# Performance work log

Hardware: AMD Instinct MI355X
Metric: run time of the kernel (lower is better)

Reference implementation:

```python
import jax, jax.numpy as jnp
import numpy as np

WIN = 7            # window side -> K2 = 49
DIM = 512          # channel dim C
HEADS = 16
E = DIM // HEADS   # embed_dim / head_dim = 32
SCALE = E ** -0.5


def _rel_pos_index(wh, ww):
    coords = np.stack(np.meshgrid(np.arange(wh), np.arange(ww), indexing='ij'))  # [2, wh, ww]
    cf = coords.reshape(2, -1)                      # [2, K2]
    rel = cf[:, :, None] - cf[:, None, :]           # [2, K2, K2]
    rel = rel.transpose(1, 2, 0).astype(np.int64)   # [K2, K2, 2]
    rel[..., 0] += wh - 1
    rel[..., 1] += ww - 1
    rel[..., 0] *= 2 * ww - 1
    return rel.sum(-1)                              # [K2, K2]

RPI = jnp.asarray(_rel_pos_index(WIN, WIN))         # constant int index map


def setup_inputs() -> dict:
    key = jax.random.key(0)
    ks = jax.random.split(key, 9)
    s = 0.02
    return {
        'x':         jax.random.normal(ks[0], (2048, WIN * WIN, DIM), jnp.float32),
        'qk_w':      jax.random.normal(ks[1], (2 * DIM, DIM), jnp.float32) * s,
        'qk_b':      jnp.zeros((2 * DIM,), jnp.float32),
        'rev_v_w':   jax.random.normal(ks[2], (DIM, DIM), jnp.float32) * s,
        'rev_v_b':   jnp.zeros((DIM,), jnp.float32),
        'wg_w':      jax.random.normal(ks[3], (E * E, DIM), jnp.float32) * s,
        'proj_w':    jax.random.normal(ks[4], (DIM, DIM), jnp.float32) * s,
        'proj_b':    jnp.zeros((DIM,), jnp.float32),
        'rpb_table': jax.random.normal(ks[5], ((2 * WIN - 1) ** 2, HEADS), jnp.float32) * s,
    }


def reference(x, qk_w, qk_b, rev_v_w, rev_v_b, wg_w, proj_w, proj_b, rpb_table):
    BW, K2, C = x.shape
    # joint q/k projection: [BW, K2, 2, H, E]
    qk = (x @ qk_w.T + qk_b).reshape(BW, K2, 2, HEADS, E)
    q = qk[:, :, 0].transpose(0, 2, 1, 3) * SCALE   # [BW, H, K2, E]
    k = qk[:, :, 1].transpose(0, 2, 1, 3)           # [BW, H, K2, E]
    attn = jnp.einsum('bhqe,bhke->bhqk', q, k)      # [BW, H, K2, K2]
    # relative position bias gather: [K2, K2, H] -> [H, K2, K2]
    bias = rpb_table[RPI].transpose(2, 0, 1)
    attn = jax.nn.softmax(attn + bias[None], axis=-1)
    # reverse attention: values projected, softmax transposed (transpose_softmax=True)
    v = (x @ rev_v_w.T + rev_v_b).reshape(BW, K2, HEADS, E).transpose(0, 2, 1, 3)  # [BW, H, K2, E]
    expert_mixture = jnp.einsum('bhkq,bhke->bhqe', attn, v)   # attn^T @ v, [BW, H, K2, E]
    # hypernetwork: per-token E x E mixing matrices from the raw input
    proj_weight = (x @ wg_w.T).reshape(BW, K2, E, E)          # [BW, K2, E, E]
    em_t = expert_mixture.transpose(0, 2, 1, 3)               # [BW, K2, H, E]
    out = jnp.einsum('bkhe,bkef->bkhf', em_t, proj_weight).reshape(BW, K2, C)
    # output projection (reverse_proj); dropouts are identity (p=0)
    return out @ proj_w.T + proj_b
```

## Files before the change

### kernel.cpp

```cpp
#include <hip/hip_runtime.h>
#include <hip/hip_bf16.h>
#include <stdint.h>

typedef __attribute__((ext_vector_type(8))) short short8;
typedef __attribute__((ext_vector_type(4))) float f32x4;
typedef unsigned short u16;

#define SCALE_F 0.17677669529663687f

__device__ __forceinline__ u16 f2bf(float f){
  union { float f; unsigned u; } x; x.f = f;
  unsigned r = x.u + 0x7fffu + ((x.u >> 16) & 1u);
  return (u16)(r >> 16);
}
__device__ __forceinline__ float bf2f(u16 u){
  union { float f; unsigned u; } x; x.u = ((unsigned)u) << 16; return x.f;
}
__device__ __forceinline__ unsigned swz(unsigned base, int row, unsigned rowb, unsigned colb){
  return base + (unsigned)row * rowb + (colb ^ (((unsigned)row & 7u) << 4));
}
__device__ __forceinline__ void gll16(const void* g, void* l){
  __builtin_amdgcn_global_load_lds(
    (const __attribute__((address_space(1))) unsigned int*)(unsigned long long)(size_t)g,
    (__attribute__((address_space(3))) unsigned int*)(unsigned int)(size_t)l,
    16, 0, 0);
}

__global__ void convk(const float* __restrict__ x,
                      const float* __restrict__ qk_w, const float* __restrict__ rev_v_w,
                      const float* __restrict__ wg_w, const float* __restrict__ proj_w,
                      u16* __restrict__ ws){
  long long i8 = ((long long)blockIdx.x * 256 + threadIdx.x) * 8;
  const float* s;
  if      (i8 <  524288) s = qk_w   + i8;
  else if (i8 <  786432) s = rev_v_w + (i8 - 524288);
  else if (i8 < 1310720) s = wg_w   + (i8 - 786432);
  else if (i8 < 1572864) s = proj_w + (i8 - 1310720);
  else                   s = x      + (i8 - 1572864);
  f32x4 lo = *(const f32x4*)s, hi = *(const f32x4*)(s + 4);
  short8 v;
  v[0]=f2bf(lo[0]); v[1]=f2bf(lo[1]); v[2]=f2bf(lo[2]); v[3]=f2bf(lo[3]);
  v[4]=f2bf(hi[0]); v[5]=f2bf(hi[1]); v[6]=f2bf(hi[2]); v[7]=f2bf(hi[3]);
  *(short8*)(ws + i8) = v;
}

template<int NT, int F32OUT>
__global__ __launch_bounds__(256, 2)
void gemm128(const u16* __restrict__ A, int lda,
             const u16* __restrict__ B,
             const float* __restrict__ b0, const float* __restrict__ b1,
             void* __restrict__ Cg, int ldc){
  __shared__ __align__(16) unsigned char sm[32768];
  const int tid = threadIdx.x, wave = tid >> 6, lane = tid & 63;
  const int l15 = lane & 15, lg = lane >> 4;
  const int nwg = gridDim.x, bidr = blockIdx.x;
  const int q8 = nwg >> 3, r8 = nwg & 7, xc = bidr & 7, oo = bidr >> 3;
  const int wg = (xc < r8 ? xc * (q8 + 1) : r8 * (q8 + 1) + (xc - r8) * q8) + oo;
  const int bm = wg / NT, bn = wg % NT;
  const int wm = wave >> 1, wn = wave & 1;
  const f32x4 zf = {0.f, 0.f, 0.f, 0.f};
  f32x4 acc[4][4];
#pragma unroll
  for (int mt=0; mt<4; mt++)
#pragma unroll
    for (int nt=0; nt<4; nt++) acc[mt][nt] = zf;

  const u16* Ab = A + (size_t)bm * 128 * lda;
  const u16* Bb = B + (size_t)bn * 128 * 512;
  const int r0 = ((wave*4)*64 + lane) >> 3;

  for (int ks = 0; ks < 8; ks++){
#pragma unroll
    for (int it = 0; it < 4; it++){
      int c = (wave*4 + it)*64 + lane;
      int r = c >> 3, cc = c & 7;
      int sc = cc ^ (r & 7);
      gll16(Ab + (size_t)r*lda + ks*64 + sc*8, sm + (unsigned)(wave*4 + it)*1024u);
      gll16(Bb + (size_t)r*512 + ks*64 + sc*8, sm + 16384u + (unsigned)(wave*4 + it)*1024u);
    }
    __syncthreads();
#pragma unroll
    for (int kk = 0; kk < 2; kk++){
      short8 aq[4], bq[4];
#pragma unroll
      for (int mt=0; mt<4; mt++){
        int r = wm*64 + mt*16 + l15;
        aq[mt] = *(const short8*)(sm + (unsigned)r*128u + (((unsigned)(kk*64 + lg*16)) ^ (((unsigned)r & 7u) << 4)));
      }
#pragma unroll
      for (int nt=0; nt<4; nt++){
        int r = wn*64 + nt*16 + l15;
        bq[nt] = *(const short8*)(sm + 16384u + (unsigned)r*128u + (((unsigned)(kk*64 + lg*16)) ^ (((unsigned)r & 7u) << 4)));
      }
#pragma unroll
      for (int mt=0; mt<4; mt++)
#pragma unroll
        for (int nt=0; nt<4; nt++)
          acc[mt][nt] = __builtin_amdgcn_mfma_f32_16x16x32_bf16(aq[mt], bq[nt], acc[mt][nt], 0, 0, 0);
    }
    __syncthreads();
  }
  (void)r0;

  float bia[4];
#pragma unroll
  for (int nt=0; nt<4; nt++){
    int n = bn*128 + wn*64 + nt*16 + l15;
    if (F32OUT) bia[nt] = b0[n];
    else        bia[nt] = (n < 1024) ? b0[n] : (n < 1536 ? b1[n - 1024] : 0.f);
  }

  if (!F32OUT){
#pragma unroll
    for (int mt=0; mt<4; mt++)
#pragma unroll
      for (int nt=0; nt<4; nt++)
#pragma unroll
        for (int i=0; i<4; i++){
          int row = wm*64 + mt*16 + lg*4 + i;
          unsigned colb = (unsigned)((wn*64 + nt*16 + l15) * 2);
          *(u16*)(sm + (unsigned)row*256u + (colb ^ (((unsigned)row & 7u) << 4))) = f2bf(acc[mt][nt][i] + bia[nt]);
        }
    __syncthreads();
    u16* Co = (u16*)Cg;
#pragma unroll
    for (int it=0; it<8; it++){
      int c = it*256 + tid;
      int r = c >> 4, cc = c & 15;
      short8 v = *(const short8*)(sm + (unsigned)r*256u + (((unsigned)(cc*16)) ^ (((unsigned)r & 7u) << 4)));
      *(short8*)(Co + (size_t)(bm*128 + r)*ldc + bn*128 + cc*8) = v;
    }
  } else {
    float* Co = (float*)Cg;
#pragma unroll
    for (int half=0; half<2; half++){
      if (wm == half){
#pragma unroll
        for (int mt=0; mt<4; mt++)
#pragma unroll
          for (int nt=0; nt<4; nt++)
#pragma unroll
            for (int i=0; i<4; i++){
              int row = mt*16 + lg*4 + i;
              unsigned colb = (unsigned)((wn*64 + nt*16 + l15) * 4);
              *(float*)(sm + (unsigned)row*512u + (colb ^ (((unsigned)row & 7u) << 4))) = acc[mt][nt][i] + bia[nt];
            }
      }
      __syncthreads();
#pragma unroll
      for (int it=0; it<8; it++){
        int c = it*256 + tid;
        int r = c >> 5, cc = c & 31;
        f32x4 v = *(const f32x4*)(sm + (unsigned)r*512u + (((unsigned)(cc*16)) ^ (((unsigned)r & 7u) << 4)));
        *(f32x4*)(Co + (size_t)(bm*128 + half*64 + r)*ldc + bn*128 + cc*4) = v;
      }
      __syncthreads();
    }
  }
}

__global__ __launch_bounds__(512, 2)
void attn_k(const u16* __restrict__ qkv, const float* __restrict__ rpb,
            u16* __restrict__ em){
  __shared__ __align__(16) unsigned char pt[50176];
  const int tid = threadIdx.x, wave = tid >> 6, lane = tid & 63;
  const int l15 = lane & 15, lg = lane >> 4;
  const size_t wb = (size_t)blockIdx.x * 49;
  const u16* base = qkv + wb * 2560;
  u16* emb = em + wb * 512;
  unsigned char* ptb = pt + (unsigned)wave * 6272u;
  const f32x4 zf = {0.f, 0.f, 0.f, 0.f};

  for (int hp = 0; hp < 2; hp++){
    const int h = wave + hp*8;
    short8 aq[4], bq[4];
#pragma unroll
    for (int mt=0; mt<4; mt++){
      int r = mt*16 + l15; if (r > 48) r = 48;
      aq[mt] = *(const short8*)(base + (size_t)r*2560 + h*32 + lg*8);
    }
#pragma unroll
    for (int nt=0; nt<4; nt++){
      int kt = nt*16 + l15; if (kt > 48) kt = 48;
      bq[nt] = *(const short8*)(base + (size_t)kt*2560 + 512 + h*32 + lg*8);
    }
    f32x4 s[4][4];
#pragma unroll
    for (int mt=0; mt<4; mt++)
#pragma unroll
      for (int nt=0; nt<4; nt++) s[mt][nt] = zf;
#pragma unroll
    for (int mt=0; mt<4; mt++)
#pragma unroll
      for (int nt=0; nt<4; nt++)
        s[mt][nt] = __builtin_amdgcn_mfma_f32_16x16x32_bf16(aq[mt], bq[nt], s[mt][nt], 0, 0, 0);
#pragma unroll
    for (int mt=0; mt<4; mt++)
#pragma unroll
      for (int nt=0; nt<4; nt++)
#pragma unroll
        for (int i=0; i<4; i++){
          int q  = mt*16 + lg*4 + i;
          int kt = nt*16 + l15;
          float v = s[mt][nt][i] * SCALE_F;
          if (kt < 49){
            int qc = (q > 48) ? 48 : q;
            int qi = qc / 7, qj = qc - qi*7;
            int ki = kt / 7, kj = kt - ki*7;
            int idx = (qi - ki + 6)*13 + (qj - kj + 6);
            v += rpb[idx*16 + h];
          } else v = -1e30f;
          s[mt][nt][i] = v;
        }
#pragma unroll
    for (int mt=0; mt<4; mt++)
#pragma unroll
      for (int i=0; i<4; i++){
        float m = fmaxf(fmaxf(s[mt][0][i], s[mt][1][i]), fmaxf(s[mt][2][i], s[mt][3][i]));
        m = fmaxf(m, __shfl_xor(m, 1)); m = fmaxf(m, __shfl_xor(m, 2));
        m = fmaxf(m, __shfl_xor(m, 4)); m = fmaxf(m, __shfl_xor(m, 8));
        float sum = 0.f;
#pragma unroll
        for (int nt=0; nt<4; nt++){ float e = __expf(s[mt][nt][i] - m); s[mt][nt][i] = e; sum += e; }
        sum += __shfl_xor(sum, 1); sum += __shfl_xor(sum, 2);
        sum += __shfl_xor(sum, 4); sum += __shfl_xor(sum, 8);
        float inv = 1.0f / sum;
#pragma unroll
        for (int nt=0; nt<4; nt++) s[mt][nt][i] *= inv;
      }
#pragma unroll
    for (int mt=0; mt<4; mt++)
#pragma unroll
      for (int nt=0; nt<4; nt++)
#pragma unroll
        for (int i=0; i<4; i++){
          int q  = mt*16 + lg*4 + i;
          int kt = nt*16 + l15;
          if (kt < 49){
            u16 val = (q < 49) ? f2bf(s[mt][nt][i]) : (u16)0;
            *(u16*)(ptb + (unsigned)kt*128u + (((unsigned)(q*2)) ^ (((unsigned)kt & 7u) << 4))) = val;
          }
        }
    f32x4 emv[4][2];
#pragma unroll
    for (int mt=0; mt<4; mt++)
#pragma unroll
      for (int nt=0; nt<2; nt++) emv[mt][nt] = zf;
#pragma unroll
    for (int kk=0; kk<2; kk++){
      short8 pa[4];
#pragma unroll
      for (int mt=0; mt<4; mt++){
        int r = mt*16 + l15; if (r > 48) r = 48;
        pa[mt] = *(const short8*)(ptb + (unsigned)r*128u + (((unsigned)(kk*64 + lg*16)) ^ (((unsigned)r & 7u) << 4)));
      }
      short8 vb[2];
#pragma unroll
      for (int nt=0; nt<2; nt++){
        int ch = 1024 + h*32 + nt*16 + l15;
#pragma unroll
        for (int j=0; j<8; j++){
          int kt = kk*32 + lg*8 + j; if (kt > 48) kt = 48;
          vb[nt][j] = *(const short*)(base + (size_t)kt*2560 + ch);
        }
      }
#pragma unroll
      for (int mt=0; mt<4; mt++)
#pragma unroll
        for (int nt=0; nt<2; nt++)
          emv[mt][nt] = __builtin_amdgcn_mfma_f32_16x16x32_bf16(pa[mt], vb[nt], emv[mt][nt], 0, 0, 0);
    }
#pragma unroll
    for (int mt=0; mt<4; mt++)
#pragma unroll
      for (int nt=0; nt<2; nt++)
#pragma unroll
        for (int i=0; i<4; i++){
          int q = mt*16 + lg*4 + i;
          if (q < 49)
            emb[(size_t)q*512 + h*32 + nt*16 + l15] = f2bf(emv[mt][nt][i]);
        }
  }
}

__global__ __launch_bounds__(512, 2)
void hyper_k(const u16* __restrict__ qkvpw, u16* __restrict__ em){
  const int tid = threadIdx.x, wave = tid >> 6, lane = tid & 63;
  const int l15 = lane & 15, lg = lane >> 4;
  const size_t t = (size_t)blockIdx.x * 8 + wave;
  const u16* pwt = qkvpw + t*2560 + 1536;
  u16* emt = em + t*512;
  const f32x4 zf = {0.f, 0.f, 0.f, 0.f};
  short8 ea = *(const short8*)(emt + l15*32 + lg*8);
  f32x4 o[2];
#pragma unroll
  for (int nt=0; nt<2; nt++){
    short8 pb;
#pragma unroll
    for (int j=0; j<8; j++){
      int e = lg*8 + j;
      pb[j] = *(const short*)(pwt + e*32 + nt*16 + l15);
    }
    o[nt] = __builtin_amdgcn_mfma_f32_16x16x32_bf16(ea, pb, zf, 0, 0, 0);
  }
#pragma unroll
  for (int nt=0; nt<2; nt++)
#pragma unroll
    for (int i=0; i<4; i++){
      int h = lg*4 + i;
      emt[h*32 + nt*16 + l15] = f2bf(o[nt][i]);
    }
}

#define LDS_X   0u
#define LDS_V   50176u
#define LDS_QK  100352u
#define LDS_RPB 150528u
#define LDS_PW  50176u
#define LDS_EM  0u
#define LDS_TOTAL 155936

__device__ __forceinline__ void gemm_strip(const unsigned char* ldsp, unsigned abase,
    const u16* __restrict__ W, int wrow0, int l15, int lg, f32x4 acc[4][4]){
  for (int kk = 0; kk < 16; kk++){
    short8 bq[4];
#pragma unroll
    for (int nt = 0; nt < 4; nt++){
      const u16* p = W + (size_t)(wrow0 + nt*16 + l15) * 512 + kk*32 + lg*8;
      bq[nt] = *(const short8*)p;
    }
    short8 aq[4];
#pragma unroll
    for (int mt = 0; mt < 4; mt++){
      int r = mt*16 + l15; if (r > 48) r = 48;
      aq[mt] = *(const short8*)(ldsp + swz(abase, r, 1024u, (unsigned)(kk*64 + lg*16)));
    }
#pragma unroll
    for (int mt = 0; mt < 4; mt++)
#pragma unroll
      for (int nt = 0; nt < 4; nt++)
        acc[mt][nt] = __builtin_amdgcn_mfma_f32_16x16x32_bf16(aq[mt], bq[nt], acc[mt][nt], 0, 0, 0);
  }
}

__global__ void conv_w4(const float* __restrict__ a, const float* __restrict__ b,
                        const float* __restrict__ c, const float* __restrict__ d,
                        u16* __restrict__ o){
  int i = blockIdx.x * 256 + threadIdx.x;
  if (i < 524288)        o[i] = f2bf(a[i]);
  else if (i < 786432)   o[i] = f2bf(b[i - 524288]);
  else if (i < 1310720)  o[i] = f2bf(c[i - 786432]);
  else                   o[i] = f2bf(d[i - 1310720]);
}

__launch_bounds__(512, 2)
__global__ void wa_main(
    const float* __restrict__ x, const float* __restrict__ qk_b,
    const float* __restrict__ rev_v_b, const float* __restrict__ proj_b,
    const float* __restrict__ rpb,
    const u16* __restrict__ Wqk, const u16* __restrict__ Wv,
    const u16* __restrict__ Wwg, const u16* __restrict__ Wproj,
    float* __restrict__ out){
  __shared__ __align__(16) unsigned char ldsp[LDS_TOTAL];
  const int tid  = threadIdx.x;
  const int wave = tid >> 6, lane = tid & 63, l15 = lane & 15, lg = lane >> 4;
  const int b = blockIdx.x;
  const float* xb = x + (size_t)b * 49 * 512;
  const f32x4 zf = {0.f, 0.f, 0.f, 0.f};
  for (int i = tid; i < 169*16; i += 512)
    *(u16*)(ldsp + LDS_RPB + i*2) = f2bf(rpb[i]);
  for (int ch = tid; ch < 49*64; ch += 512){
    int r = ch >> 6, c8 = ch & 63;
    const f32x4* s = (const f32x4*)(xb + r*512 + c8*8);
    f32x4 lo = s[0], hi = s[1];
    short8 v;
    v[0]=f2bf(lo[0]); v[1]=f2bf(lo[1]); v[2]=f2bf(lo[2]); v[3]=f2bf(lo[3]);
    v[4]=f2bf(hi[0]); v[5]=f2bf(hi[1]); v[6]=f2bf(hi[2]); v[7]=f2bf(hi[3]);
    *(short8*)(ldsp + swz(LDS_X, r, 1024u, (unsigned)(c8*16))) = v;
  }
  __syncthreads();
  {
    f32x4 acc[4][4];
#pragma unroll
    for (int mt=0; mt<4; mt++)
#pragma unroll
      for (int nt=0; nt<4; nt++) acc[mt][nt] = zf;
    gemm_strip(ldsp, LDS_X, Wv, wave*64, l15, lg, acc);
#pragma unroll
    for (int nt=0; nt<4; nt++){
      int ch = wave*64 + nt*16 + l15;
      float bias = rev_v_b[ch];
#pragma unroll
      for (int mt=0; mt<4; mt++)
#pragma unroll
        for (int i=0; i<4; i++){
          int r = mt*16 + lg*4 + i;
          if (r < 49)
            *(u16*)(ldsp + swz(LDS_V, r, 1024u, (unsigned)(ch*2))) = f2bf(acc[mt][nt][i] + bias);
        }
    }
  }
  auto qk_pass = [&](int p){
    f32x4 acc[4][4];
#pragma unroll
    for (int mt=0; mt<4; mt++)
#pragma unroll
      for (int nt=0; nt<4; nt++) acc[mt][nt] = zf;
    int wrow0 = (wave < 4) ? (p*256 + wave*64) : (512 + p*256 + (wave-4)*64);
    gemm_strip(ldsp, LDS_X, Wqk, wrow0, l15, lg, acc);
#pragma unroll
    for (int nt=0; nt<4; nt++){
      int ch  = wrow0 + nt*16 + l15;
      int col = wave*64 + nt*16 + l15;
      float bias = qk_b[ch];
#pragma unroll
      for (int mt=0; mt<4; mt++)
#pragma unroll
        for (int i=0; i<4; i++){
          int r = mt*16 + lg*4 + i;
          if (r < 49)
            *(u16*)(ldsp + swz(LDS_QK, r, 1024u, (unsigned)(col*2))) = f2bf(acc[mt][nt][i] + bias);
        }
    }
  };
  auto attn_pass = [&](int p, f32x4 (&em)[4][2]){
    const int h = p*8 + wave;
    f32x4 s[4][4];
#pragma unroll
    for (int mt=0; mt<4; mt++)
#pragma unroll
      for (int nt=0; nt<4; nt++) s[mt][nt] = zf;
    short8 aq[4], bq[4];
#pragma unroll
    for (int mt=0; mt<4; mt++){
      int r = mt*16 + l15; if (r > 48) r = 48;
      aq[mt] = *(const short8*)(ldsp + swz(LDS_QK, r, 1024u, (unsigned)(wave*64 + lg*16)));
    }
#pragma unroll
    for (int nt=0; nt<4; nt++){
      int kt = nt*16 + l15; if (kt > 48) kt = 48;
      bq[nt] = *(const short8*)(ldsp + swz(LDS_QK, kt, 1024u, (unsigned)(512 + wave*64 + lg*16)));
    }
#pragma unroll
    for (int mt=0; mt<4; mt++)
#pragma unroll
      for (int nt=0; nt<4; nt++)
        s[mt][nt] = __builtin_amdgcn_mfma_f32_16x16x32_bf16(aq[mt], bq[nt], s[mt][nt], 0, 0, 0);
#pragma unroll
    for (int mt=0; mt<4; mt++)
#pragma unroll
      for (int nt=0; nt<4; nt++)
#pragma unroll
        for (int i=0; i<4; i++){
          int q  = mt*16 + lg*4 + i;
          int kt = nt*16 + l15;
          float v = s[mt][nt][i] * SCALE_F;
          if (kt < 49){
            int qc = (q > 48) ? 48 : q;
            int qi = qc / 7, qj = qc - qi*7;
            int ki = kt / 7, kj = kt - ki*7;
            int idx = (qi - ki + 6)*13 + (qj - kj + 6);
            v += bf2f(*(const u16*)(ldsp + LDS_RPB + (idx*16 + h)*2));
          } else v = -1e30f;
          s[mt][nt][i] = v;
        }
#pragma unroll
    for (int mt=0; mt<4; mt++)
#pragma unroll
      for (int i=0; i<4; i++){
        float m = fmaxf(fmaxf(s[mt][0][i], s[mt][1][i]), fmaxf(s[mt][2][i], s[mt][3][i]));
        m = fmaxf(m, __shfl_xor(m, 1)); m = fmaxf(m, __shfl_xor(m, 2));
        m = fmaxf(m, __shfl_xor(m, 4)); m = fmaxf(m, __shfl_xor(m, 8));
        float sum = 0.f;
#pragma unroll
        for (int nt=0; nt<4; nt++){ float e = __expf(s[mt][nt][i] - m); s[mt][nt][i] = e; sum += e; }
        sum += __shfl_xor(sum, 1); sum += __shfl_xor(sum, 2);
        sum += __shfl_xor(sum, 4); sum += __shfl_xor(sum, 8);
        float inv = 1.0f / sum;
#pragma unroll
        for (int nt=0; nt<4; nt++) s[mt][nt][i] *= inv;
      }
    __syncthreads();
    const unsigned ptb = LDS_QK + (unsigned)wave * 6272u;
#pragma unroll
    for (int mt=0; mt<4; mt++)
#pragma unroll
      for (int nt=0; nt<4; nt++)
#pragma unroll
        for (int i=0; i<4; i++){
          int q  = mt*16 + lg*4 + i;
          int kt = nt*16 + l15;
          if (kt < 49){
            u16 val = (q < 49) ? f2bf(s[mt][nt][i]) : (u16)0;
            *(u16*)(ldsp + ptb + (unsigned)kt*128u + (((unsigned)(q*2)) ^ (((unsigned)kt & 7u) << 4))) = val;
          }
        }
#pragma unroll
    for (int kk=0; kk<2; kk++){
      short8 pa[4];
#pragma unroll
      for (int mt=0; mt<4; mt++){
        int r = mt*16 + l15; if (r > 48) r = 48;
        pa[mt] = *(const short8*)(ldsp + ptb + (unsigned)r*128u + (((unsigned)(kk*64 + lg*16)) ^ (((unsigned)r & 7u) << 4)));
      }
      short8 vb[2];
#pragma unroll
      for (int nt=0; nt<2; nt++){
        int ch = h*32 + nt*16 + l15;
#pragma unroll
        for (int j=0; j<8; j++){
          int kt = kk*32 + lg*8 + j; if (kt > 48) kt = 48;
          vb[nt][j] = *(const short*)(ldsp + swz(LDS_V, kt, 1024u, (unsigned)(ch*2)));
        }
      }
#pragma unroll
      for (int mt=0; mt<4; mt++)
#pragma unroll
        for (int nt=0; nt<2; nt++)
          em[mt][nt] = __builtin_amdgcn_mfma_f32_16x16x32_bf16(pa[mt], vb[nt], em[mt][nt], 0, 0, 0);
    }
  };
  f32x4 em0[4][2], em1[4][2];
#pragma unroll
  for (int mt=0; mt<4; mt++)
#pragma unroll
    for (int nt=0; nt<2; nt++){ em0[mt][nt] = zf; em1[mt][nt] = zf; }
  qk_pass(0);
  __syncthreads();
  attn_pass(0, em0);
  __syncthreads();
  qk_pass(1);
  __syncthreads();
  attn_pass(1, em1);
  __syncthreads();
  for (int nh = 0; nh < 2; nh++){
    f32x4 acc[4][4];
#pragma unroll
    for (int mt=0; mt<4; mt++)
#pragma unroll
      for (int nt=0; nt<4; nt++) acc[mt][nt] = zf;
    int n0 = nh*512 + wave*64;
    gemm_strip(ldsp, LDS_X, Wwg, n0, l15, lg, acc);
#pragma unroll
    for (int nt=0; nt<4; nt++){
      int n  = n0 + nt*16 + l15;
      int pc = (n & 31)*32 + (n >> 5);
      unsigned cb = ((unsigned)(pc*2)) ^ (((unsigned)n & 7u) << 4);
#pragma unroll
      for (int mt=0; mt<4; mt++)
#pragma unroll
        for (int i=0; i<4; i++){
          int r = mt*16 + lg*4 + i;
          if (r < 49)
            *(u16*)(ldsp + LDS_PW + (unsigned)r*2048u + cb) = f2bf(acc[mt][nt][i]);
        }
    }
  }
  __syncthreads();
  auto em_store = [&](f32x4 (&em)[4][2], int h){
#pragma unroll
    for (int mt=0; mt<4; mt++)
#pragma unroll
      for (int nt=0; nt<2; nt++)
#pragma unroll
        for (int i=0; i<4; i++){
          int q = mt*16 + lg*4 + i;
          if (q < 49){
            int ch = h*32 + nt*16 + l15;
            *(u16*)(ldsp + swz(LDS_EM, q, 1024u, (unsigned)(ch*2))) = f2bf(em[mt][nt][i]);
          }
        }
  };
  em_store(em0, wave);
  em_store(em1, 8 + wave);
  __syncthreads();
  for (int t = wave; t < 49; t += 8){
    short8 ea = *(const short8*)(ldsp + swz(LDS_EM, t, 1024u, (unsigned)(l15*64 + lg*16)));
    f32x4 o[2];
#pragma unroll
    for (int nt=0; nt<2; nt++){
      int f = nt*16 + l15;
      short8 pb = *(const short8*)(ldsp + LDS_PW + (unsigned)t*2048u +
                    (((unsigned)((f*32 + lg*8)*2)) ^ (((unsigned)f & 7u) << 4)));
      o[nt] = __builtin_amdgcn_mfma_f32_16x16x32_bf16(ea, pb, zf, 0, 0, 0);
    }
#pragma unroll
    for (int nt=0; nt<2; nt++)
#pragma unroll
      for (int i=0; i<4; i++){
        int h2 = lg*4 + i;
        int ch = h2*32 + nt*16 + l15;
        *(u16*)(ldsp + swz(LDS_EM, t, 1024u, (unsigned)(ch*2))) = f2bf(o[nt][i]);
      }
  }
  __syncthreads();
  {
    f32x4 acc[4][4];
#pragma unroll
    for (int mt=0; mt<4; mt++)
#pragma unroll
      for (int nt=0; nt<4; nt++) acc[mt][nt] = zf;
    gemm_strip(ldsp, LDS_EM, Wproj, wave*64, l15, lg, acc);
    float* ob = out + (size_t)b * 49 * 512;
#pragma unroll
    for (int nt=0; nt<4; nt++){
      int n = wave*64 + nt*16 + l15;
      float bias = proj_b[n];
#pragma unroll
      for (int mt=0; mt<4; mt++)
#pragma unroll
        for (int i=0; i<4; i++){
          int r = mt*16 + lg*4 + i;
          if (r < 49) ob[r*512 + n] = acc[mt][nt][i] + bias;
        }
    }
  }
}

extern "C" void kernel_launch(void* const* d_in, const int* in_sizes, int n_in,
                              void* d_out, int out_size, void* d_ws, size_t ws_size,
                              hipStream_t stream){
  const float* x       = (const float*)d_in[0];
  const float* qk_w    = (const float*)d_in[1];
  const float* qk_b    = (const float*)d_in[2];
  const float* rev_v_w = (const float*)d_in[3];
  const float* rev_v_b = (const float*)d_in[4];
  const float* wg_w    = (const float*)d_in[5];
  const float* proj_w  = (const float*)d_in[6];
  const float* proj_b  = (const float*)d_in[7];
  const float* rpb     = (const float*)d_in[8];
  u16* ws = (u16*)d_ws;

  const unsigned long long BASE = 105906176ULL;
  int C = 0;
  for (int cand : {2048, 1024, 512, 256, 128}){
    if (BASE + (unsigned long long)cand * 301056ULL <= ws_size){ C = cand; break; }
  }
  if (C == 0){
    conv_w4<<<6144, 256, 0, stream>>>(qk_w, rev_v_w, wg_w, proj_w, ws);
    wa_main<<<2048, 512, 0, stream>>>(x, qk_b, rev_v_b, proj_b, rpb,
        ws, ws + 524288, ws + 786432, ws + 1310720, (float*)d_out);
    return;
  }

  u16* Wcat  = ws;
  u16* Wproj = ws + 1310720;
  u16* xb    = ws + 1572864;
  u16* qkvpw = ws + 52953088ULL;
  u16* em    = qkvpw + (size_t)C * 49 * 2560;

  convk<<<25856, 256, 0, stream>>>(x, qk_w, rev_v_w, wg_w, proj_w, ws);

  const int nch = 2048 / C;
  const int mt128 = C * 49 / 128;
  for (int ch = 0; ch < nch; ch++){
    size_t t0 = (size_t)ch * C * 49;
    gemm128<20, 0><<<mt128 * 20, 256, 0, stream>>>(xb + t0*512, 512, Wcat,
        qk_b, rev_v_b, qkvpw, 2560);
    attn_k<<<C, 512, 0, stream>>>(qkvpw, rpb, em);
    hyper_k<<<C * 49 / 8, 512, 0, stream>>>(qkvpw, em);
    gemm128<4, 1><<<mt128 * 4, 256, 0, stream>>>(em, 512, Wproj,
        proj_b, (const float*)nullptr, (float*)d_out + t0*512, 512);
  }
}
```

Measured before the change: 812.6 us.

## Fuse attention and hypernetwork mixing into one kernel with LDS-staged V and bias

Measured after the change: 691.0 us. 15.0% less time.

```diff
diff --git a/kernel.cpp b/kernel.cpp
--- a/kernel.cpp
+++ b/kernel.cpp
@@ -67,7 +67,6 @@
 
   const u16* Ab = A + (size_t)bm * 128 * lda;
   const u16* Bb = B + (size_t)bn * 128 * 512;
-  const int r0 = ((wave*4)*64 + lane) >> 3;
 
   for (int ks = 0; ks < 8; ks++){
 #pragma unroll
@@ -100,7 +99,6 @@
     }
     __syncthreads();
   }
-  (void)r0;
 
   float bia[4];
 #pragma unroll
@@ -160,18 +158,27 @@
 }
 
 __global__ __launch_bounds__(512, 2)
-void attn_k(const u16* __restrict__ qkv, const float* __restrict__ rpb,
-            u16* __restrict__ em){
-  __shared__ __align__(16) unsigned char pt[50176];
+void attn_fused(const u16* __restrict__ qkv, const float* __restrict__ rpb,
+                u16* __restrict__ o1){
+  __shared__ __align__(16) unsigned char lds[105760];
+  const unsigned L_V = 0u, L_PT = 50176u, L_RPB = 100352u;
   const int tid = threadIdx.x, wave = tid >> 6, lane = tid & 63;
   const int l15 = lane & 15, lg = lane >> 4;
   const size_t wb = (size_t)blockIdx.x * 49;
   const u16* base = qkv + wb * 2560;
-  u16* emb = em + wb * 512;
-  unsigned char* ptb = pt + (unsigned)wave * 6272u;
+  unsigned char* ptb = lds + L_PT + (unsigned)wave * 6272u;
   const f32x4 zf = {0.f, 0.f, 0.f, 0.f};
 
-  for (int hp = 0; hp < 2; hp++){
+  for (int i = tid; i < 2704; i += 512)
+    *(u16*)(lds + L_RPB + i*2) = f2bf(rpb[i]);
+  for (int c = tid; c < 49*64; c += 512){
+    int r = c >> 6, c8 = c & 63;
+    short8 v = *(const short8*)(base + (size_t)r*2560 + 1024 + c8*8);
+    *(short8*)(lds + swz(L_V, r, 1024u, (unsigned)(c8*16))) = v;
+  }
+  __syncthreads();
+
+  auto attn_pass = [&](int hp, f32x4 (&em)[4][2]){
     const int h = wave + hp*8;
     short8 aq[4], bq[4];
 #pragma unroll
@@ -208,7 +215,7 @@
             int qi = qc / 7, qj = qc - qi*7;
             int ki = kt / 7, kj = kt - ki*7;
             int idx = (qi - ki + 6)*13 + (qj - kj + 6);
-            v += rpb[idx*16 + h];
+            v += bf2f(*(const u16*)(lds + L_RPB + (idx*16 + h)*2));
           } else v = -1e30f;
           s[mt][nt][i] = v;
         }
@@ -241,11 +248,6 @@
             *(u16*)(ptb + (unsigned)kt*128u + (((unsigned)(q*2)) ^ (((unsigned)kt & 7u) << 4))) = val;
           }
         }
-    f32x4 emv[4][2];
-#pragma unroll
-    for (int mt=0; mt<4; mt++)
-#pragma unroll
-      for (int nt=0; nt<2; nt++) emv[mt][nt] = zf;
 #pragma unroll
     for (int kk=0; kk<2; kk++){
       short8 pa[4];
@@ -257,19 +259,31 @@
       short8 vb[2];
 #pragma unroll
       for (int nt=0; nt<2; nt++){
-        int ch = 1024 + h*32 + nt*16 + l15;
+        int ch = h*32 + nt*16 + l15;
 #pragma unroll
         for (int j=0; j<8; j++){
           int kt = kk*32 + lg*8 + j; if (kt > 48) kt = 48;
-          vb[nt][j] = *(const short*)(base + (size_t)kt*2560 + ch);
+          vb[nt][j] = *(const short*)(lds + swz(L_V, kt, 1024u, (unsigned)(ch*2)));
         }
       }
 #pragma unroll
       for (int mt=0; mt<4; mt++)
 #pragma unroll
         for (int nt=0; nt<2; nt++)
-          emv[mt][nt] = __builtin_amdgcn_mfma_f32_16x16x32_bf16(pa[mt], vb[nt], emv[mt][nt], 0, 0, 0);
-    }
+          em[mt][nt] = __builtin_amdgcn_mfma_f32_16x16x32_bf16(pa[mt], vb[nt], em[mt][nt], 0, 0, 0);
+    }
+  };
+
+  f32x4 em0[4][2], em1[4][2];
+#pragma unroll
+  for (int mt=0; mt<4; mt++)
+#pragma unroll
+    for (int nt=0; nt<2; nt++){ em0[mt][nt] = zf; em1[mt][nt] = zf; }
+  attn_pass(0, em0);
+  attn_pass(1, em1);
+  __syncthreads();
+
+  auto em_store = [&](f32x4 (&em)[4][2], int h){
 #pragma unroll
     for (int mt=0; mt<4; mt++)
 #pragma unroll
@@ -277,39 +291,53 @@
 #pragma unroll
         for (int i=0; i<4; i++){
           int q = mt*16 + lg*4 + i;
-          if (q < 49)
-            emb[(size_t)q*512 + h*32 + nt*16 + l15] = f2bf(emv[mt][nt][i]);
-        }
-  }
-}
-
-__global__ __launch_bounds__(512, 2)
-void hyper_k(const u16* __restrict__ qkvpw, u16* __restrict__ em){
-  const int tid = threadIdx.x, wave = tid >> 6, lane = tid & 63;
-  const int l15 = lane & 15, lg = lane >> 4;
-  const size_t t = (size_t)blockIdx.x * 8 + wave;
-  const u16* pwt = qkvpw + t*2560 + 1536;
-  u16* emt = em + t*512;
-  const f32x4 zf = {0.f, 0.f, 0.f, 0.f};
-  short8 ea = *(const short8*)(emt + l15*32 + lg*8);
-  f32x4 o[2];
-#pragma unroll
-  for (int nt=0; nt<2; nt++){
-    short8 pb;
-#pragma unroll
-    for (int j=0; j<8; j++){
-      int e = lg*8 + j;
-      pb[j] = *(const short*)(pwt + e*32 + nt*16 + l15);
-    }
-    o[nt] = __builtin_amdgcn_mfma_f32_16x16x32_bf16(ea, pb, zf, 0, 0, 0);
-  }
-#pragma unroll
-  for (int nt=0; nt<2; nt++)
-#pragma unroll
-    for (int i=0; i<4; i++){
-      int h = lg*4 + i;
-      emt[h*32 + nt*16 + l15] = f2bf(o[nt][i]);
-    }
+          if (q < 49){
+            int ch = h*32 + nt*16 + l15;
+            *(u16*)(lds + swz(L_V, q, 1024u, (unsigned)(ch*2))) = f2bf(em[mt][nt][i]);
+          }
+        }
+  };
+  em_store(em0, wave);
+  em_store(em1, 8 + wave);
+  __syncthreads();
+
+  for (int t = wave; t < 49; t += 8){
+    const u16* pwt = base + (size_t)t*2560 + 1536;
+#pragma unroll
+    for (int rd = 0; rd < 2; rd++){
+      int i8 = (rd*64 + lane)*8;
+      short8 v = *(const short8*)(pwt + i8);
+      int e = i8 >> 5, f0 = i8 & 31;
+#pragma unroll
+      for (int jj = 0; jj < 8; jj++){
+        int f = f0 + jj;
+        *(u16*)(ptb + (unsigned)f*64u + (((unsigned)(e*2)) ^ (((unsigned)f & 3u) << 4))) = (u16)v[jj];
+      }
+    }
+    short8 ea = *(const short8*)(lds + swz(L_V, t, 1024u, (unsigned)(l15*64 + lg*16)));
+    f32x4 o[2];
+#pragma unroll
+    for (int nt=0; nt<2; nt++){
+      int f = nt*16 + l15;
+      short8 pb = *(const short8*)(ptb + (unsigned)f*64u + (((unsigned)(lg*16)) ^ (((unsigned)f & 3u) << 4)));
+      o[nt] = __builtin_amdgcn_mfma_f32_16x16x32_bf16(ea, pb, zf, 0, 0, 0);
+    }
+#pragma unroll
+    for (int nt=0; nt<2; nt++)
+#pragma unroll
+      for (int i=0; i<4; i++){
+        int ch = (lg*4 + i)*32 + nt*16 + l15;
+        *(u16*)(lds + swz(L_V, t, 1024u, (unsigned)(ch*2))) = f2bf(o[nt][i]);
+      }
+  }
+  __syncthreads();
+
+  u16* ob = o1 + wb * 512;
+  for (int c = tid; c < 49*64; c += 512){
+    int r = c >> 6, c8 = c & 63;
+    short8 v = *(const short8*)(lds + swz(L_V, r, 1024u, (unsigned)(c8*16)));
+    *(short8*)(ob + (size_t)r*512 + c8*8) = v;
+  }
 }
 
 #define LDS_X   0u
@@ -647,7 +675,7 @@
   u16* Wproj = ws + 1310720;
   u16* xb    = ws + 1572864;
   u16* qkvpw = ws + 52953088ULL;
-  u16* em    = qkvpw + (size_t)C * 49 * 2560;
+  u16* o1    = qkvpw + (size_t)C * 49 * 2560;
 
   convk<<<25856, 256, 0, stream>>>(x, qk_w, rev_v_w, wg_w, proj_w, ws);
 
@@ -657,9 +685,9 @@
     size_t t0 = (size_t)ch * C * 49;
     gemm128<20, 0><<<mt128 * 20, 256, 0, stream>>>(xb + t0*512, 512, Wcat,
         qk_b, rev_v_b, qkvpw, 2560);
-    attn_k<<<C, 512, 0, stream>>>(qkvpw, rpb, em);
-    hyper_k<<<C * 49 / 8, 512, 0, stream>>>(qkvpw, em);
-    gemm128<4, 1><<<mt128 * 4, 256, 0, stream>>>(em, 512, Wproj,
+    attn_fused<<<C, 512, 0, stream>>>(qkvpw, rpb, o1);
+    gemm128<4, 1><<<mt128 * 4, 256, 0, stream>>>(o1, 512, Wproj,
         proj_b, (const float*)nullptr, (float*)d_out + t0*512, 512);
   }
-}
+  (void)Wcat; (void)Wproj;
+}
```

## Split attention per head-half, stage V and bias in LDS, transpose hyper weights

Applied to the files above, without the earlier changes.

Result: faster. 666.2 us (-18.0%).

```diff
diff --git a/kernel.cpp b/kernel.cpp
--- a/kernel.cpp
+++ b/kernel.cpp
@@ -67,7 +67,6 @@
 
   const u16* Ab = A + (size_t)bm * 128 * lda;
   const u16* Bb = B + (size_t)bn * 128 * 512;
-  const int r0 = ((wave*4)*64 + lane) >> 3;
 
   for (int ks = 0; ks < 8; ks++){
 #pragma unroll
@@ -100,7 +99,6 @@
     }
     __syncthreads();
   }
-  (void)r0;
 
   float bia[4];
 #pragma unroll
@@ -159,157 +157,183 @@
   }
 }
 
-__global__ __launch_bounds__(512, 2)
-void attn_k(const u16* __restrict__ qkv, const float* __restrict__ rpb,
-            u16* __restrict__ em){
-  __shared__ __align__(16) unsigned char pt[50176];
+__global__ __launch_bounds__(512, 4)
+void attn_half(const u16* __restrict__ qkv, const float* __restrict__ rpb,
+               u16* __restrict__ em){
+  __shared__ __align__(16) unsigned char lds[77968];
+  const unsigned L_V = 0u, L_PT = 25088u, L_RPB = 75264u;
   const int tid = threadIdx.x, wave = tid >> 6, lane = tid & 63;
   const int l15 = lane & 15, lg = lane >> 4;
-  const size_t wb = (size_t)blockIdx.x * 49;
-  const u16* base = qkv + wb * 2560;
-  u16* emb = em + wb * 512;
-  unsigned char* ptb = pt + (unsigned)wave * 6272u;
+  const int bid = blockIdx.x, win = bid >> 1, hf = bid & 1;
+  const u16* base = qkv + (size_t)win * 49 * 2560;
+  u16* emb = em + (size_t)win * 49 * 512 + hf * 256;
+  unsigned char* ptb = lds + L_PT + (unsigned)wave * 6272u;
+  const int h = hf*8 + wave;
   const f32x4 zf = {0.f, 0.f, 0.f, 0.f};
 
-  for (int hp = 0; hp < 2; hp++){
-    const int h = wave + hp*8;
-    short8 aq[4], bq[4];
+  for (int i = tid; i < 169*8; i += 512){
+    int idx = i >> 3, hh = i & 7;
+    *(u16*)(lds + L_RPB + i*2) = f2bf(rpb[idx*16 + hf*8 + hh]);
+  }
+  for (int c = tid; c < 49*32; c += 512){
+    int r = c >> 5, c8 = c & 31;
+    short8 v = *(const short8*)(base + (size_t)r*2560 + 1024 + hf*256 + c8*8);
+    *(short8*)(lds + swz(L_V, r, 512u, (unsigned)(c8*16))) = v;
+  }
+  __syncthreads();
+
+  short8 aq[4], bq[4];
+#pragma unroll
+  for (int mt=0; mt<4; mt++){
+    int r = mt*16 + l15; if (r > 48) r = 48;
+    aq[mt] = *(const short8*)(base + (size_t)r*2560 + h*32 + lg*8);
+  }
+#pragma unroll
+  for (int nt=0; nt<4; nt++){
+    int kt = nt*16 + l15; if (kt > 48) kt = 48;
+    bq[nt] = *(const short8*)(base + (size_t)kt*2560 + 512 + h*32 + lg*8);
+  }
+  f32x4 s[4][4];
+#pragma unroll
+  for (int mt=0; mt<4; mt++)
+#pragma unroll
+    for (int nt=0; nt<4; nt++) s[mt][nt] = zf;
+#pragma unroll
+  for (int mt=0; mt<4; mt++)
+#pragma unroll
+    for (int nt=0; nt<4; nt++)
+      s[mt][nt] = __builtin_amdgcn_mfma_f32_16x16x32_bf16(aq[mt], bq[nt], s[mt][nt], 0, 0, 0);
+#pragma unroll
+  for (int mt=0; mt<4; mt++)
+#pragma unroll
+    for (int nt=0; nt<4; nt++)
+#pragma unroll
+      for (int i=0; i<4; i++){
+        int q  = mt*16 + lg*4 + i;
+        int kt = nt*16 + l15;
+        float v = s[mt][nt][i] * SCALE_F;
+        if (kt < 49){
+          int qc = (q > 48) ? 48 : q;
+          int qi = qc / 7, qj = qc - qi*7;
+          int ki = kt / 7, kj = kt - ki*7;
+          int idx = (qi - ki + 6)*13 + (qj - kj + 6);
+          v += bf2f(*(const u16*)(lds + L_RPB + (idx*8 + wave)*2));
+        } else v = -1e30f;
+        s[mt][nt][i] = v;
+      }
+#pragma unroll
+  for (int mt=0; mt<4; mt++)
+#pragma unroll
+    for (int i=0; i<4; i++){
+      float m = fmaxf(fmaxf(s[mt][0][i], s[mt][1][i]), fmaxf(s[mt][2][i], s[mt][3][i]));
+      m = fmaxf(m, __shfl_xor(m, 1)); m = fmaxf(m, __shfl_xor(m, 2));
+      m = fmaxf(m, __shfl_xor(m, 4)); m = fmaxf(m, __shfl_xor(m, 8));
+      float sum = 0.f;
+#pragma unroll
+      for (int nt=0; nt<4; nt++){ float e = __expf(s[mt][nt][i] - m); s[mt][nt][i] = e; sum += e; }
+      sum += __shfl_xor(sum, 1); sum += __shfl_xor(sum, 2);
+      sum += __shfl_xor(sum, 4); sum += __shfl_xor(sum, 8);
+      float inv = 1.0f / sum;
+#pragma unroll
+      for (int nt=0; nt<4; nt++) s[mt][nt][i] *= inv;
+    }
+#pragma unroll
+  for (int mt=0; mt<4; mt++)
+#pragma unroll
+    for (int nt=0; nt<4; nt++)
+#pragma unroll
+      for (int i=0; i<4; i++){
+        int q  = mt*16 + lg*4 + i;
+        int kt = nt*16 + l15;
+        if (kt < 49){
+          u16 val = (q < 49) ? f2bf(s[mt][nt][i]) : (u16)0;
+          *(u16*)(ptb + (unsigned)kt*128u + (((unsigned)(q*2)) ^ (((unsigned)kt & 7u) << 4))) = val;
+        }
+      }
+  f32x4 emv[4][2];
+#pragma unroll
+  for (int mt=0; mt<4; mt++)
+#pragma unroll
+    for (int nt=0; nt<2; nt++) emv[mt][nt] = zf;
+#pragma unroll
+  for (int kk=0; kk<2; kk++){
+    short8 pa[4];
 #pragma unroll
     for (int mt=0; mt<4; mt++){
       int r = mt*16 + l15; if (r > 48) r = 48;
-      aq[mt] = *(const short8*)(base + (size_t)r*2560 + h*32 + lg*8);
-    }
-#pragma unroll
-    for (int nt=0; nt<4; nt++){
-      int kt = nt*16 + l15; if (kt > 48) kt = 48;
-      bq[nt] = *(const short8*)(base + (size_t)kt*2560 + 512 + h*32 + lg*8);
-    }
-    f32x4 s[4][4];
-#pragma unroll
-    for (int mt=0; mt<4; mt++)
-#pragma unroll
-      for (int nt=0; nt<4; nt++) s[mt][nt] = zf;
-#pragma unroll
-    for (int mt=0; mt<4; mt++)
-#pragma unroll
-      for (int nt=0; nt<4; nt++)
-        s[mt][nt] = __builtin_amdgcn_mfma_f32_16x16x32_bf16(aq[mt], bq[nt], s[mt][nt], 0, 0, 0);
-#pragma unroll
-    for (int mt=0; mt<4; mt++)
-#pragma unroll
-      for (int nt=0; nt<4; nt++)
-#pragma unroll
-        for (int i=0; i<4; i++){
-          int q  = mt*16 + lg*4 + i;
-          int kt = nt*16 + l15;
-          float v = s[mt][nt][i] * SCALE_F;
-          if (kt < 49){
-            int qc = (q > 48) ? 48 : q;
-            int qi = qc / 7, qj = qc - qi*7;
-            int ki = kt / 7, kj = kt - ki*7;
-            int idx = (qi - ki + 6)*13 + (qj - kj + 6);
-            v += rpb[idx*16 + h];
-          } else v = -1e30f;
-          s[mt][nt][i] = v;
-        }
-#pragma unroll
-    for (int mt=0; mt<4; mt++)
+      pa[mt] = *(const short8*)(ptb + (unsigned)r*128u + (((unsigned)(kk*64 + lg*16)) ^ (((unsigned)r & 7u) << 4)));
+    }
+    short8 vb[2];
+#pragma unroll
+    for (int nt=0; nt<2; nt++){
+      int chl = wave*32 + nt*16 + l15;
+#pragma unroll
+      for (int j=0; j<8; j++){
+        int kt = kk*32 + lg*8 + j; if (kt > 48) kt = 48;
+        vb[nt][j] = *(const short*)(lds + swz(L_V, kt, 512u, (unsigned)(chl*2)));
+      }
+    }
+#pragma unroll
+    for (int mt=0; mt<4; mt++)
+#pragma unroll
+      for (int nt=0; nt<2; nt++)
+        emv[mt][nt] = __builtin_amdgcn_mfma_f32_16x16x32_bf16(pa[mt], vb[nt], emv[mt][nt], 0, 0, 0);
+  }
+#pragma unroll
+  for (int mt=0; mt<4; mt++)
+#pragma unroll
+    for (int nt=0; nt<2; nt++)
 #pragma unroll
       for (int i=0; i<4; i++){
-        float m = fmaxf(fmaxf(s[mt][0][i], s[mt][1][i]), fmaxf(s[mt][2][i], s[mt][3][i]));
-        m = fmaxf(m, __shfl_xor(m, 1)); m = fmaxf(m, __shfl_xor(m, 2));
-        m = fmaxf(m, __shfl_xor(m, 4)); m = fmaxf(m, __shfl_xor(m, 8));
-        float sum = 0.f;
-#pragma unroll
-        for (int nt=0; nt<4; nt++){ float e = __expf(s[mt][nt][i] - m); s[mt][nt][i] = e; sum += e; }
-        sum += __shfl_xor(sum, 1); sum += __shfl_xor(sum, 2);
-        sum += __shfl_xor(sum, 4); sum += __shfl_xor(sum, 8);
-        float inv = 1.0f / sum;
-#pragma unroll
-        for (int nt=0; nt<4; nt++) s[mt][nt][i] *= inv;
-      }
-#pragma unroll
-    for (int mt=0; mt<4; mt++)
-#pragma unroll
-      for (int nt=0; nt<4; nt++)
-#pragma unroll
-        for (int i=0; i<4; i++){
-          int q  = mt*16 + lg*4 + i;
-          int kt = nt*16 + l15;
-          if (kt < 49){
-            u16 val = (q < 49) ? f2bf(s[mt][nt][i]) : (u16)0;
-            *(u16*)(ptb + (unsigned)kt*128u + (((unsigned)(q*2)) ^ (((unsigned)kt & 7u) << 4))) = val;
-          }
-        }
-    f32x4 emv[4][2];
-#pragma unroll
-    for (int mt=0; mt<4; mt++)
-#pragma unroll
-      for (int nt=0; nt<2; nt++) emv[mt][nt] = zf;
-#pragma unroll
-    for (int kk=0; kk<2; kk++){
-      short8 pa[4];
-#pragma unroll
-      for (int mt=0; mt<4; mt++){
-        int r = mt*16 + l15; if (r > 48) r = 48;
-        pa[mt] = *(const short8*)(ptb + (unsigned)r*128u + (((unsigned)(kk*64 + lg*16)) ^ (((unsigned)r & 7u) << 4)));
-      }
-      short8 vb[2];
-#pragma unroll
-      for (int nt=0; nt<2; nt++){
-        int ch = 1024 + h*32 + nt*16 + l15;
-#pragma unroll
-        for (int j=0; j<8; j++){
-          int kt = kk*32 + lg*8 + j; if (kt > 48) kt = 48;
-          vb[nt][j] = *(const short*)(base + (size_t)kt*2560 + ch);
-        }
-      }
-#pragma unroll
-      for (int mt=0; mt<4; mt++)
-#pragma unroll
-        for (int nt=0; nt<2; nt++)
-          emv[mt][nt] = __builtin_amdgcn_mfma_f32_16x16x32_bf16(pa[mt], vb[nt], emv[mt][nt], 0, 0, 0);
-    }
-#pragma unroll
-    for (int mt=0; mt<4; mt++)
-#pragma unroll
-      for (int nt=0; nt<2; nt++)
-#pragma unroll
-        for (int i=0; i<4; i++){
-          int q = mt*16 + lg*4 + i;
-          if (q < 49)
-            emb[(size_t)q*512 + h*32 + nt*16 + l15] = f2bf(emv[mt][nt][i]);
-        }
-  }
-}
-
-__global__ __launch_bounds__(512, 2)
-void hyper_k(const u16* __restrict__ qkvpw, u16* __restrict__ em){
+        int q = mt*16 + lg*4 + i;
+        if (q < 49)
+          emb[(size_t)q*512 + wave*32 + nt*16 + l15] = f2bf(emv[mt][nt][i]);
+      }
+}
+
+__global__ __launch_bounds__(512, 4)
+void hyper2(const u16* __restrict__ qkvpw, const u16* __restrict__ em,
+            u16* __restrict__ o1){
+  __shared__ __align__(16) unsigned char lds[16384];
   const int tid = threadIdx.x, wave = tid >> 6, lane = tid & 63;
   const int l15 = lane & 15, lg = lane >> 4;
+  unsigned char* pwb = lds + (unsigned)wave * 2048u;
   const size_t t = (size_t)blockIdx.x * 8 + wave;
   const u16* pwt = qkvpw + t*2560 + 1536;
-  u16* emt = em + t*512;
+  const u16* emt = em + t*512;
   const f32x4 zf = {0.f, 0.f, 0.f, 0.f};
+
+#pragma unroll
+  for (int rd = 0; rd < 2; rd++){
+    int i8 = (rd*64 + lane)*8;
+    short8 v = *(const short8*)(pwt + i8);
+    int e = i8 >> 5, f0 = i8 & 31;
+#pragma unroll
+    for (int jj = 0; jj < 8; jj++){
+      int f = f0 + jj;
+      *(u16*)(pwb + (unsigned)f*64u + (((unsigned)(e*2)) ^ (((unsigned)f & 3u) << 4))) = (u16)v[jj];
+    }
+  }
   short8 ea = *(const short8*)(emt + l15*32 + lg*8);
+  __syncthreads();
   f32x4 o[2];
 #pragma unroll
   for (int nt=0; nt<2; nt++){
-    short8 pb;
-#pragma unroll
-    for (int j=0; j<8; j++){
-      int e = lg*8 + j;
-      pb[j] = *(const short*)(pwt + e*32 + nt*16 + l15);
-    }
+    int f = nt*16 + l15;
+    short8 pb = *(const short8*)(pwb + (unsigned)f*64u + (((unsigned)(lg*16)) ^ (((unsigned)f & 3u) << 4)));
     o[nt] = __builtin_amdgcn_mfma_f32_16x16x32_bf16(ea, pb, zf, 0, 0, 0);
   }
+  __syncthreads();
 #pragma unroll
   for (int nt=0; nt<2; nt++)
 #pragma unroll
     for (int i=0; i<4; i++){
-      int h = lg*4 + i;
-      emt[h*32 + nt*16 + l15] = f2bf(o[nt][i]);
-    }
+      int ch = (lg*4 + i)*32 + nt*16 + l15;
+      *(u16*)(pwb + (unsigned)ch*2u) = f2bf(o[nt][i]);
+    }
+  __syncthreads();
+  short8 v = *(const short8*)(pwb + (unsigned)lane*16u);
+  *(short8*)(o1 + t*512 + lane*8) = v;
 }
 
 #define LDS_X   0u
@@ -633,8 +657,8 @@
 
   const unsigned long long BASE = 105906176ULL;
   int C = 0;
-  for (int cand : {2048, 1024, 512, 256, 128}){
-    if (BASE + (unsigned long long)cand * 301056ULL <= ws_size){ C = cand; break; }
+  for (int cand : {512, 1024, 2048, 256, 128}){
+    if (BASE + (unsigned long long)cand * 351232ULL <= ws_size){ C = cand; break; }
   }
   if (C == 0){
     conv_w4<<<6144, 256, 0, stream>>>(qk_w, rev_v_w, wg_w, proj_w, ws);
@@ -647,7 +671,8 @@
   u16* Wproj = ws + 1310720;
   u16* xb    = ws + 1572864;
   u16* qkvpw = ws + 52953088ULL;
-  u16* em    = qkvpw + (size_t)C * 49 * 2560;
+  u16* o1    = qkvpw + (size_t)C * 49 * 2560;
+  u16* em    = o1 + (size_t)C * 49 * 512;
 
   convk<<<25856, 256, 0, stream>>>(x, qk_w, rev_v_w, wg_w, proj_w, ws);
 
@@ -657,9 +682,10 @@
     size_t t0 = (size_t)ch * C * 49;
     gemm128<20, 0><<<mt128 * 20, 256, 0, stream>>>(xb + t0*512, 512, Wcat,
         qk_b, rev_v_b, qkvpw, 2560);
-    attn_k<<<C, 512, 0, stream>>>(qkvpw, rpb, em);
-    hyper_k<<<C * 49 / 8, 512, 0, stream>>>(qkvpw, em);
-    gemm128<4, 1><<<mt128 * 4, 256, 0, stream>>>(em, 512, Wproj,
+    attn_half<<<2 * C, 512, 0, stream>>>(qkvpw, rpb, em);
+    hyper2<<<C * 49 / 8, 512, 0, stream>>>(qkvpw, em, o1);
+    gemm128<4, 1><<<mt128 * 4, 256, 0, stream>>>(o1, 512, Wproj,
         proj_b, (const float*)nullptr, (float*)d_out + t0*512, 512);
   }
-}
+  (void)Wcat; (void)Wproj;
+}
```
